# Kernel optimization log

Measured on AMD Instinct MI355X. Metric: run time of the kernel, lower is better.

Reference implementation:

```python
import jax, jax.numpy as jnp
import numpy as np

FEAT = 256
HID = FEAT // 2
N_KEYS = 2          # output_keys = ["energy_0", "energy_1"]
N_MOLS = 2000
ATOMS_PER_MOL = 100
N_ATOMS = N_MOLS * ATOMS_PER_MOL
LOG2 = 0.6931471805599453


def shifted_softplus(x):
    # NFF's shifted softplus: softplus(x) - log(2)
    return jax.nn.softplus(x) - LOG2


def setup_inputs() -> dict:
    key = jax.random.key(0)
    ks = jax.random.split(key, 6)
    s_i = jax.random.normal(ks[0], (N_ATOMS, FEAT), dtype=jnp.float32)
    xyz = jax.random.normal(ks[1], (N_ATOMS, 3), dtype=jnp.float32)
    num_atoms = jnp.full((N_MOLS,), ATOMS_PER_MOL, dtype=jnp.int64)
    # Per-key MLP params stacked over keys: Linear(F->H), act, Linear(H->1)
    W1 = jax.random.normal(ks[2], (N_KEYS, FEAT, HID), dtype=jnp.float32) / np.sqrt(FEAT)
    b1 = jnp.zeros((N_KEYS, HID), dtype=jnp.float32)
    W2 = jax.random.normal(ks[3], (N_KEYS, HID), dtype=jnp.float32) / np.sqrt(HID)
    b2 = jnp.zeros((N_KEYS,), dtype=jnp.float32)
    return {"s_i": s_i, "xyz": xyz, "num_atoms": num_atoms,
            "W1": W1, "b1": b1, "W2": W2, "b2": b2}


def reference(s_i, xyz, num_atoms, W1, b1, W2, b2):
    n_mols = num_atoms.shape[0]
    # segment id per atom, replacing the torch.split(...)+per-chunk sum loop
    seg = jnp.repeat(jnp.arange(n_mols), num_atoms,
                     total_repeat_length=s_i.shape[0])        # [N]
    # per-key MLP: [K,N,H] hidden, [K,N] scalar output per atom
    h = shifted_softplus(jnp.einsum('nf,kfh->knh', s_i, W1) + b1[:, None, :])
    val = jnp.einsum('knh,kh->kn', h, W2) + b2[:, None]       # [K, N]
    # fused segment-sum pooling -> per-molecule scalars
    pooled = jax.ops.segment_sum(val.T, seg, num_segments=n_mols)  # [M, K]
    return pooled.T                                            # [K, M]
```

## Files before the change

### kernel.cpp

```cpp
#include <hip/hip_runtime.h>

#define FEAT 256
#define HID 128
#define NKEYS 2

typedef __bf16 bf16x8 __attribute__((ext_vector_type(8)));
typedef float f32x16 __attribute__((ext_vector_type(16)));

union Frag {
    bf16x8 v;
    unsigned u[4];
    uint4 q;
};

__device__ __forceinline__ unsigned pack_bf16_2(float f0, float f1) {
    unsigned u0 = __float_as_uint(f0) + 0x8000u;
    unsigned u1 = __float_as_uint(f1) + 0x8000u;
    return __builtin_amdgcn_perm(u1, u0, 0x07060302u);
}

__device__ __forceinline__ float ssp(float x) {
    float sp = __logf(1.0f + __expf(x));
    sp = (x > 15.0f) ? x : sp;
    return sp - 0.69314718056f;
}

__device__ __forceinline__ int find_mol(const int* off, int n_mols, int g) {
    int lo = 0, hi = n_mols;
    while (hi - lo > 1) {
        int mid = (lo + hi) >> 1;
        if (off[mid] <= g) lo = mid; else hi = mid;
    }
    return lo;
}

__device__ __forceinline__ void gload_lds16(const float* g, void* l) {
    __builtin_amdgcn_global_load_lds(
        (const __attribute__((address_space(1))) unsigned int*)g,
        (__attribute__((address_space(3))) unsigned int*)l,
        16, 0, 0);
}

__global__ void prep_kernel(const void* __restrict__ num_atoms_raw,
                            const float* __restrict__ W1,
                            int n_mols, int n_atoms,
                            int* __restrict__ off,
                            unsigned short* __restrict__ Bp,
                            float* __restrict__ out, int out_n) {
    if (blockIdx.x > 0) {
        int idx = (blockIdx.x - 1) * 256 + threadIdx.x;
        int c = idx >> 8;
        int k = idx & 255;
        int key = c >> 7, j = c & 127;
        float f = W1[(size_t)key * FEAT * HID + (size_t)k * HID + j];
        unsigned u = __float_as_uint(f);
        unsigned r = (u + 0x7FFFu + ((u >> 16) & 1u)) >> 16;
        Bp[(size_t)c * FEAT + k] = (unsigned short)r;
        return;
    }
    for (int i = threadIdx.x; i < out_n; i += 256) out[i] = 0.0f;

    __shared__ long long tsum[256];
    __shared__ int csum[256];
    int tid = threadIdx.x;
    const int* a32 = (const int*)num_atoms_raw;
    const long long* a64 = (const long long*)num_atoms_raw;
    int chunk = (n_mols + 255) >> 8;
    int lo = tid * chunk;
    if (lo > n_mols) lo = n_mols;
    int hi = lo + chunk;
    if (hi > n_mols) hi = n_mols;

    long long s32 = 0;
    for (int i = lo; i < hi; ++i) s32 += (long long)a32[i];
    tsum[tid] = s32;
    __syncthreads();
    #pragma unroll
    for (int d = 128; d > 0; d >>= 1) {
        if (tid < d) tsum[tid] += tsum[tid + d];
        __syncthreads();
    }
    int mode = (tsum[0] == (long long)n_atoms) ? 0 : 1;
    long long s = s32;
    if (mode) {
        s = 0;
        for (int i = lo; i < hi; ++i) s += a64[i];
    }
    int v = (int)s;
    csum[tid] = v;
    __syncthreads();
    #pragma unroll
    for (int d = 1; d < 256; d <<= 1) {
        int t = (tid >= d) ? csum[tid - d] : 0;
        __syncthreads();
        csum[tid] += t;
        __syncthreads();
    }
    int run = csum[tid] - v;
    for (int i = lo; i < hi; ++i) {
        off[i] = run;
        run += mode ? (int)a64[i] : a32[i];
    }
    if (hi >= n_mols) off[n_mols] = run;
}

__global__ __launch_bounds__(512, 4)
void gemm_fused(const float* __restrict__ A,
                const unsigned short* __restrict__ Bp,
                const float* __restrict__ b1,
                const float* __restrict__ W2,
                const float* __restrict__ b2,
                const int* __restrict__ off,
                float* __restrict__ out,
                int n_atoms, int n_mols, int ntiles, int stride) {
    __shared__ uint4  ldsA[2][1024];
    __shared__ int    offlds[2048];
    __shared__ float  part[2][8][64];
    __shared__ int    rowmol[2][64];
    __shared__ float  molacc[2][NKEYS][4];

    const int tid  = threadIdx.x;
    const int lane = tid & 63;
    const int wid  = tid >> 6;
    const int l31  = lane & 31;
    const int half = lane >> 5;

    const bool lds_ok = (n_mols + 1) <= 2048;
    if (lds_ok) ((int4*)offlds)[tid] = ((const int4*)off)[tid];
    if (tid < 2 * NKEYS * 4) {
        int b = tid >> 3;
        molacc[b][(tid >> 2) & 1][tid & 3] = 0.0f;
    }
    const float b2k0 = b2[0], b2k1 = b2[1];
    const int c0 = wid * 32 + l31;
    const unsigned short* bb = Bp + (size_t)c0 * FEAT + half * 8;
    const float b1c = b1[c0];
    const float w2c = W2[c0];
    const int rB = l31 + 32;
    const int x  = l31 & 15;

    int t = blockIdx.x;
    int cur = 0;

    auto stage = [&](int tile, int c, int buf) {
        const int m0s = tile * 64;
        #pragma unroll
        for (int i = 0; i < 2; ++i) {
            const int pos = wid * 128 + i * 64;
            const int r   = (pos >> 4) + (lane >> 4);
            const int u   = (lane & 15) ^ (r & 15);
            int gr = m0s + r;
            if (gr > n_atoms - 1) gr = n_atoms - 1;
            gload_lds16(A + (size_t)gr * FEAT + c * 64 + u * 4,
                        (void*)(&ldsA[buf][pos]));
        }
    };

    stage(t, 0, 0);
    __syncthreads();

    int it = 0;
    for (; t < ntiles; t += stride, ++it) {
        const int tp = it & 1;
        const int m0 = t * 64;
        f32x16 acc0 = 0.0f, acc1 = 0.0f;

        #pragma unroll
        for (int c = 0; c < 4; ++c) {
            Frag bw[4];
            #pragma unroll
            for (int j = 0; j < 4; ++j)
                bw[j].q = *(const uint4*)(bb + c * 64 + j * 16);
            __builtin_amdgcn_sched_barrier(0);

            const bool last = (c == 3) && (t + stride >= ntiles);
            if (!last) {
                const int nt = (c < 3) ? t : (t + stride);
                stage(nt, (c + 1) & 3, cur ^ 1);
            }

            if (c == 0 && tid < 64) {
                int gm = m0 + tid;
                if (gm > n_atoms - 1) gm = n_atoms - 1;
                rowmol[tp][tid] = lds_ok ? find_mol(offlds, n_mols, gm)
                                         : find_mol(off, n_mols, gm);
            }

            const uint4* lbuf = ldsA[cur];
            #pragma unroll
            for (int ks = 0; ks < 4; ++ks) {
                const int u0 = ks * 4 + half * 2;
                const int us = u0 ^ x;
                uint4 lo0 = lbuf[l31 * 16 + us];
                uint4 hi0 = lbuf[l31 * 16 + (us ^ 1)];
                uint4 lo1 = lbuf[rB  * 16 + us];
                uint4 hi1 = lbuf[rB  * 16 + (us ^ 1)];
                const float4 fl0 = *(const float4*)&lo0;
                const float4 fh0 = *(const float4*)&hi0;
                const float4 fl1 = *(const float4*)&lo1;
                const float4 fh1 = *(const float4*)&hi1;
                Frag a0, a1;
                a0.u[0] = pack_bf16_2(fl0.x, fl0.y);
                a0.u[1] = pack_bf16_2(fl0.z, fl0.w);
                a0.u[2] = pack_bf16_2(fh0.x, fh0.y);
                a0.u[3] = pack_bf16_2(fh0.z, fh0.w);
                a1.u[0] = pack_bf16_2(fl1.x, fl1.y);
                a1.u[1] = pack_bf16_2(fl1.z, fl1.w);
                a1.u[2] = pack_bf16_2(fh1.x, fh1.y);
                a1.u[3] = pack_bf16_2(fh1.z, fh1.w);
                acc0 = __builtin_amdgcn_mfma_f32_32x32x16_bf16(a0.v, bw[ks].v, acc0, 0, 0, 0);
                acc1 = __builtin_amdgcn_mfma_f32_32x32x16_bf16(a1.v, bw[ks].v, acc1, 0, 0, 0);
            }

            if (c == 3) {
                #pragma unroll
                for (int rt = 0; rt < 2; ++rt) {
                    const f32x16& Ac = rt ? acc1 : acc0;
                    #pragma unroll
                    for (int r = 0; r < 16; ++r) {
                        float v = ssp(Ac[r] + b1c) * w2c;
                        v += __shfl_xor(v, 1);
                        v += __shfl_xor(v, 2);
                        v += __shfl_xor(v, 4);
                        v += __shfl_xor(v, 8);
                        v += __shfl_xor(v, 16);
                        if (l31 == r) {
                            int row = rt * 32 + (r & 3) + 8 * (r >> 2) + 4 * half;
                            part[tp][wid][row] = v;
                        }
                    }
                }
            }

            __syncthreads();
            cur ^= 1;

            if (c == 3) {
                if (it > 0 && tid < NKEYS * 4) {
                    const int pp = tp ^ 1;
                    int k = tid >> 2, ml = tid & 3;
                    int mol = rowmol[pp][0] + ml;
                    if (mol < n_mols) {
                        float v = molacc[pp][k][ml];
                        if (v != 0.0f) atomicAdd(&out[(size_t)k * n_mols + mol], v);
                        molacc[pp][k][ml] = 0.0f;
                    }
                }
                if (tid < NKEYS * 64) {
                    int k = tid >> 6, r = tid & 63;
                    int gm = m0 + r;
                    if (gm < n_atoms) {
                        float val = part[tp][4 * k][r] + part[tp][4 * k + 1][r]
                                  + part[tp][4 * k + 2][r] + part[tp][4 * k + 3][r]
                                  + (k ? b2k1 : b2k0);
                        int mol = rowmol[tp][r];
                        int ml  = mol - rowmol[tp][0];
                        if (ml < 4) atomicAdd(&molacc[tp][k][ml], val);
                        else        atomicAdd(&out[(size_t)k * n_mols + mol], val);
                    }
                }
            }
        }
    }

    __syncthreads();
    const int tpl = (it - 1) & 1;
    if (tid < NKEYS * 4) {
        int k = tid >> 2, ml = tid & 3;
        int mol = rowmol[tpl][0] + ml;
        if (mol < n_mols) {
            float v = molacc[tpl][k][ml];
            if (v != 0.0f) atomicAdd(&out[(size_t)k * n_mols + mol], v);
        }
    }
}

extern "C" void kernel_launch(void* const* d_in, const int* in_sizes, int n_in,
                              void* d_out, int out_size, void* d_ws, size_t ws_size,
                              hipStream_t stream) {
    const float* s_i      = (const float*)d_in[0];
    const void*  num_atoms = d_in[2];
    const float* W1 = (const float*)d_in[3];
    const float* b1 = (const float*)d_in[4];
    const float* W2 = (const float*)d_in[5];
    const float* b2 = (const float*)d_in[6];
    int n_atoms = in_sizes[0] / FEAT;
    int n_mols  = in_sizes[2];
    float* out = (float*)d_out;

    int* off = (int*)d_ws;
    size_t off_bytes = (((size_t)(n_mols + 1) * 4) + 255) & ~(size_t)255;
    if (off_bytes < 8192) off_bytes = 8192;
    unsigned short* Bp = (unsigned short*)((char*)d_ws + off_bytes);

    int pack_blocks = (NKEYS * HID * FEAT) / 256;
    prep_kernel<<<1 + pack_blocks, 256, 0, stream>>>(num_atoms, W1, n_mols, n_atoms,
                                                     off, Bp, out, out_size);

    int ntiles  = (n_atoms + 63) / 64;
    int nblocks = ntiles < 512 ? ntiles : 512;
    gemm_fused<<<nblocks, 512, 0, stream>>>(s_i, Bp, b1, W2, b2, off, out,
                                            n_atoms, n_mols, ntiles, nblocks);
}
```

Measured before the change: 373.0 us.

## Single-buffer epilogue state and move pooling epilogue out of the k-chunk loop

Drops the double-buffered part/rowmol/molacc shared arrays and their deferred flush of the previous tile. The activation, reduction and segment-pooling epilogue now runs after all four K chunks, followed by an immediate per-tile flush of the molecule accumulators. The row-to-molecule lookups are spread across all eight waves instead of being done only in wave 0. This saves shared memory and simplifies control flow, but adds two block-wide barriers per tile and loses the overlap of one tile's flush with the next tile's work.

```diff
diff --git a/kernel.cpp b/kernel.cpp
--- a/kernel.cpp
+++ b/kernel.cpp
@@ -115,9 +115,9 @@
                 int n_atoms, int n_mols, int ntiles, int stride) {
     __shared__ uint4  ldsA[2][1024];
     __shared__ int    offlds[2048];
-    __shared__ float  part[2][8][64];
-    __shared__ int    rowmol[2][64];
-    __shared__ float  molacc[2][NKEYS][4];
+    __shared__ float  part[8][64];
+    __shared__ int    rowmol[64];
+    __shared__ float  molacc[NKEYS][4];
 
     const int tid  = threadIdx.x;
     const int lane = tid & 63;
@@ -127,20 +127,15 @@
 
     const bool lds_ok = (n_mols + 1) <= 2048;
     if (lds_ok) ((int4*)offlds)[tid] = ((const int4*)off)[tid];
-    if (tid < 2 * NKEYS * 4) {
-        int b = tid >> 3;
-        molacc[b][(tid >> 2) & 1][tid & 3] = 0.0f;
-    }
-    const float b2k0 = b2[0], b2k1 = b2[1];
+    if (tid < NKEYS * 4) molacc[tid >> 2][tid & 3] = 0.0f;
+
     const int c0 = wid * 32 + l31;
     const unsigned short* bb = Bp + (size_t)c0 * FEAT + half * 8;
-    const float b1c = b1[c0];
-    const float w2c = W2[c0];
+    const float b1c  = b1[c0];
+    const float w2c  = W2[c0];
+    const float b2k0 = b2[0], b2k1 = b2[1];
     const int rB = l31 + 32;
     const int x  = l31 & 15;
-
-    int t = blockIdx.x;
-    int cur = 0;
 
     auto stage = [&](int tile, int c, int buf) {
         const int m0s = tile * 64;
@@ -156,12 +151,12 @@
         }
     };
 
+    int t = blockIdx.x;
+    int cur = 0;
     stage(t, 0, 0);
     __syncthreads();
 
-    int it = 0;
-    for (; t < ntiles; t += stride, ++it) {
-        const int tp = it & 1;
+    for (; t < ntiles; t += stride) {
         const int m0 = t * 64;
         f32x16 acc0 = 0.0f, acc1 = 0.0f;
 
@@ -174,23 +169,20 @@
             __builtin_amdgcn_sched_barrier(0);
 
             const bool last = (c == 3) && (t + stride >= ntiles);
-            if (!last) {
-                const int nt = (c < 3) ? t : (t + stride);
-                stage(nt, (c + 1) & 3, cur ^ 1);
-            }
-
-            if (c == 0 && tid < 64) {
-                int gm = m0 + tid;
+            if (!last) stage((c < 3) ? t : (t + stride), (c + 1) & 3, cur ^ 1);
+
+            if (c == 0 && (tid & 7) == 0) {
+                int r = tid >> 3;
+                int gm = m0 + r;
                 if (gm > n_atoms - 1) gm = n_atoms - 1;
-                rowmol[tp][tid] = lds_ok ? find_mol(offlds, n_mols, gm)
-                                         : find_mol(off, n_mols, gm);
+                rowmol[r] = lds_ok ? find_mol(offlds, n_mols, gm)
+                                   : find_mol(off, n_mols, gm);
             }
 
             const uint4* lbuf = ldsA[cur];
             #pragma unroll
             for (int ks = 0; ks < 4; ++ks) {
-                const int u0 = ks * 4 + half * 2;
-                const int us = u0 ^ x;
+                const int us = (ks * 4 + half * 2) ^ x;
                 uint4 lo0 = lbuf[l31 * 16 + us];
                 uint4 hi0 = lbuf[l31 * 16 + (us ^ 1)];
                 uint4 lo1 = lbuf[rB  * 16 + us];
@@ -212,65 +204,52 @@
                 acc1 = __builtin_amdgcn_mfma_f32_32x32x16_bf16(a1.v, bw[ks].v, acc1, 0, 0, 0);
             }
 
-            if (c == 3) {
-                #pragma unroll
-                for (int rt = 0; rt < 2; ++rt) {
-                    const f32x16& Ac = rt ? acc1 : acc0;
-                    #pragma unroll
-                    for (int r = 0; r < 16; ++r) {
-                        float v = ssp(Ac[r] + b1c) * w2c;
-                        v += __shfl_xor(v, 1);
-                        v += __shfl_xor(v, 2);
-                        v += __shfl_xor(v, 4);
-                        v += __shfl_xor(v, 8);
-                        v += __shfl_xor(v, 16);
-                        if (l31 == r) {
-                            int row = rt * 32 + (r & 3) + 8 * (r >> 2) + 4 * half;
-                            part[tp][wid][row] = v;
-                        }
-                    }
-                }
-            }
-
             __syncthreads();
             cur ^= 1;
-
-            if (c == 3) {
-                if (it > 0 && tid < NKEYS * 4) {
-                    const int pp = tp ^ 1;
-                    int k = tid >> 2, ml = tid & 3;
-                    int mol = rowmol[pp][0] + ml;
-                    if (mol < n_mols) {
-                        float v = molacc[pp][k][ml];
-                        if (v != 0.0f) atomicAdd(&out[(size_t)k * n_mols + mol], v);
-                        molacc[pp][k][ml] = 0.0f;
-                    }
+        }
+
+        #pragma unroll
+        for (int rt = 0; rt < 2; ++rt) {
+            const f32x16& Ac = rt ? acc1 : acc0;
+            #pragma unroll
+            for (int r = 0; r < 16; ++r) {
+                float v = ssp(Ac[r] + b1c) * w2c;
+                v += __shfl_xor(v, 1);
+                v += __shfl_xor(v, 2);
+                v += __shfl_xor(v, 4);
+                v += __shfl_xor(v, 8);
+                v += __shfl_xor(v, 16);
+                if (l31 == r) {
+                    int row = rt * 32 + (r & 3) + 8 * (r >> 2) + 4 * half;
+                    part[wid][row] = v;
                 }
-                if (tid < NKEYS * 64) {
-                    int k = tid >> 6, r = tid & 63;
-                    int gm = m0 + r;
-                    if (gm < n_atoms) {
-                        float val = part[tp][4 * k][r] + part[tp][4 * k + 1][r]
-                                  + part[tp][4 * k + 2][r] + part[tp][4 * k + 3][r]
-                                  + (k ? b2k1 : b2k0);
-                        int mol = rowmol[tp][r];
-                        int ml  = mol - rowmol[tp][0];
-                        if (ml < 4) atomicAdd(&molacc[tp][k][ml], val);
-                        else        atomicAdd(&out[(size_t)k * n_mols + mol], val);
-                    }
-                }
-            }
-        }
-    }
-
-    __syncthreads();
-    const int tpl = (it - 1) & 1;
-    if (tid < NKEYS * 4) {
-        int k = tid >> 2, ml = tid & 3;
-        int mol = rowmol[tpl][0] + ml;
-        if (mol < n_mols) {
-            float v = molacc[tpl][k][ml];
-            if (v != 0.0f) atomicAdd(&out[(size_t)k * n_mols + mol], v);
+            }
+        }
+        __syncthreads();
+
+        if (tid < NKEYS * 64) {
+            int k = tid >> 6, r = tid & 63;
+            int gm = m0 + r;
+            if (gm < n_atoms) {
+                float val = part[4 * k][r] + part[4 * k + 1][r]
+                          + part[4 * k + 2][r] + part[4 * k + 3][r]
+                          + (k ? b2k1 : b2k0);
+                int mol = rowmol[r];
+                int ml  = mol - rowmol[0];
+                if (ml < 4) atomicAdd(&molacc[k][ml], val);
+                else        atomicAdd(&out[(size_t)k * n_mols + mol], val);
+            }
+        }
+        __syncthreads();
+
+        if (tid < NKEYS * 4) {
+            int k = tid >> 2, ml = tid & 3;
+            int mol = rowmol[0] + ml;
+            if (mol < n_mols) {
+                float v = molacc[k][ml];
+                if (v != 0.0f) atomicAdd(&out[(size_t)k * n_mols + mol], v);
+                molacc[k][ml] = 0.0f;
+            }
         }
     }
 }
```

Result: no change. 375.5 us (+0.6%).
